# Kernel tuning notes

Measured on AMD Instinct MI355X. Metric: run time of the kernel, lower is better.

## Reference

```python
import jax, jax.numpy as jnp
import numpy as np

ITER_ROUTING = 3
FINAL_LAMBDA = 0.01
EPS = 1e-9

N = 4
CHILD_SPACE = 12
KERNEL = 3
STRIDE = 1
CHILD_CAPS = 16
PARENT_CAPS = 32
POSE = 16


def _routing_map(child_space, k, s):
    # (child_space^2, parent_space^2) binary map: child c feeds parent p.
    parent_space = (child_space - k) // s + 1
    m = np.zeros((child_space * child_space, parent_space * parent_space), np.float32)
    for pr in range(parent_space):
        for pc in range(parent_space):
            p = pr * parent_space + pc
            for r in range(k):
                for c in range(k):
                    m[(pr * s + r) * child_space + (pc * s + c), p] = 1.0
    return m


def setup_inputs() -> dict:
    key = jax.random.key(0)
    k1, k2, k3, k4 = jax.random.split(key, 4)
    parent_space = (CHILD_SPACE - KERNEL) // STRIDE + 1
    kk = KERNEL * KERNEL
    votes = jax.random.normal(k1, (N * parent_space * parent_space, kk * CHILD_CAPS, PARENT_CAPS, POSE), jnp.float32)
    acts = jax.random.uniform(k2, (N * parent_space * parent_space, kk * CHILD_CAPS, 1), dtype=jnp.float32)
    beta_v = jax.random.normal(k3, (1, 1, 1, 1, PARENT_CAPS, 1), jnp.float32)
    beta_a = jax.random.normal(k4, (1, 1, 1, 1, PARENT_CAPS, 1), jnp.float32)
    srm = jnp.asarray(_routing_map(CHILD_SPACE, KERNEL, STRIDE))
    return {"votes_ij": votes, "activations_i": acts, "beta_v": beta_v, "beta_a": beta_a,
            "spatial_routing_matrix": srm, "batch_size": N, "kk": kk}


def _em_routing(votes_ij, activations_i, beta_v, beta_a, srm, batch_size, kk):
    Nb = batch_size
    C2, P2 = srm.shape  # child_space^2, parent_space^2
    P = int(round(P2 ** 0.5))
    K_total, O, ch = votes_ij.shape[1], votes_ij.shape[2], votes_ij.shape[3]
    child_caps = K_total // kk

    votes = votes_ij.reshape(Nb, P, P, K_total, O, ch)
    act_i = activations_i.reshape(Nb, P, P, K_total, 1, 1)

    # children per parent, ascending child index (stable argsort on -1/0 values)
    cidx = jnp.argsort(-srm, axis=0)[:kk].T           # (P2, kk)
    seg = cidx.reshape(-1)                            # (P2*kk,) child id per (parent, slot)
    ppc = jnp.sum(srm, axis=1)                        # parents-per-child, (C2,)
    # init_rr: 1 / (parents_per_child * parent_caps + 1e-9), gathered per parent slot
    rr0 = (1.0 / (ppc[cidx] * O + 1e-9)).reshape(1, P, P, kk, 1, 1)
    rr = jnp.broadcast_to(rr0, (1, P, P, kk, child_caps, O)).reshape(1, P, P, K_total, O, 1)

    layer_norm_factor = 100.0 / (float(K_total) / float(O))

    def m_step(rr, it):
        lam = FINAL_LAMBDA * (1.0 - 0.95 ** (it + 1))
        rr_prime = rr * act_i                                            # (N,P,P,K,O,1)
        rr_prime_sum = jnp.sum(rr_prime, axis=-3, keepdims=True)         # (N,P,P,1,O,1)
        mean_j = jnp.sum(rr_prime * votes, axis=-3, keepdims=True) / (rr_prime_sum + EPS)
        var_j = jnp.sum(rr_prime * jnp.square(votes - mean_j), axis=-3, keepdims=True) / (rr_prime_sum + EPS)
        cost_j_h = (beta_v + 0.5 * jnp.log(var_j + EPS)) * rr_prime_sum * layer_norm_factor
        cost_j = jnp.sum(cost_j_h, axis=-1, keepdims=True)               # (N,P,P,1,O,1)
        cost_mean = jnp.mean(cost_j, axis=-2, keepdims=True)
        cost_stdv = jnp.sqrt(jnp.sum(jnp.square(cost_j - cost_mean), axis=-2, keepdims=True) / O)
        act_j = jax.nn.sigmoid(lam * (beta_a + (cost_mean - cost_j) / (cost_stdv + EPS)))
        return act_j, mean_j, var_j

    def e_step(act_j, mean_j, var_j):
        # log N(vote; mean_j, var_j) per parent + log activation
        o_p0 = -jnp.sum(jnp.square(votes - mean_j) / (2.0 * var_j), axis=-1, keepdims=True)
        o_p2 = -0.5 * jnp.sum(jnp.log(2.0 * np.pi * var_j), axis=-1, keepdims=True)
        zz = jnp.log(act_j + EPS) + o_p0 + o_p2                          # (N,P,P,K,O,1)
        # softmax over ALL parents of each child (spatial kk slots x parent_caps),
        # done via segment reductions keyed by child id (== sparse/softmax/dense of original)
        z = jnp.moveaxis(zz.reshape(Nb, P2 * kk, child_caps, O), 1, 0)   # (P2*kk, N, cc, O)
        m = jax.ops.segment_max(jnp.max(z, axis=-1), seg, num_segments=C2)  # (C2, N, cc)
        m = jnp.where(jnp.isinf(m), 0.0, m)
        e = jnp.exp(z - m[seg][..., None])
        denom = jax.ops.segment_sum(jnp.sum(e, axis=-1), seg, num_segments=C2)
        rr_new = e / denom[seg][..., None]
        return jnp.moveaxis(rr_new, 0, 1).reshape(Nb, P, P, K_total, O, 1)

    for it in range(ITER_ROUTING):
        act_j, mean_j, var_j = m_step(rr, it)
        if it < ITER_ROUTING - 1:
            rr = e_step(act_j, mean_j, var_j)

    poses_j = mean_j[:, :, :, 0]        # (N,P,P,O,16)
    activations_j = act_j[:, :, :, 0]   # (N,P,P,O,1)
    return poses_j, activations_j


def reference(votes_ij, activations_i, beta_v, beta_a, spatial_routing_matrix, batch_size, kk):
    return _em_routing(votes_ij, activations_i, beta_v, beta_a, spatial_routing_matrix, batch_size, kk)
```

## Files before the change

### kernel.cpp

```cpp
#include <hip/hip_runtime.h>
#include <math.h>

#define NB     4
#define P      10
#define P2     100
#define CS     12
#define CCAPS  16
#define KTOT   144
#define O      32
#define POSE   16
#define EPSF   1e-9f
#define LNF    22.2222222222222222f
#define LOG2PI 1.83787706640934548f

#define RRN (NB*P2*KTOT*O)

__device__ float g_rr[RRN];
__device__ float g_zz[RRN];

__device__ __forceinline__ int npar(int x) {
    int a = x + 1, b = CS - x;
    int m = a < 3 ? a : 3;
    return m < b ? m : b;
}

template<bool FIRST, bool LAST>
__global__ __launch_bounds__(512)
void mstep_kernel(const float* __restrict__ votes,
                  const float* __restrict__ acts,
                  const float* __restrict__ beta_v,
                  const float* __restrict__ beta_a,
                  float* __restrict__ out, float lam)
{
    __shared__ __align__(16) float rr_lds[KTOT * O];
    __shared__ float act_lds[KTOT];
    __shared__ __align__(16) float mean_lds[512];
    __shared__ __align__(16) float i2v_lds[512];
    __shared__ float cost_lds[O];
    __shared__ float slv_lds[O];
    __shared__ float zpre_lds[O];
    __shared__ float actj_lds[O];

    const int tid = threadIdx.x;
    const int kq  = tid >> 7;
    const int q   = tid & 127;
    const int o   = q >> 2;
    const int c4  = q & 3;
    const int bp  = blockIdx.x;
    const int p   = bp % P2;
    const int pr  = p / P, pc = p % P;

    if (tid < KTOT) act_lds[tid] = acts[bp * KTOT + tid];
    __syncthreads();

    if (FIRST) {
        for (int f = tid; f < KTOT * O / 4; f += 512) {
            int k = f >> 3;
            int kslot = k >> 4;
            int kr = kslot / 3, kc = kslot % 3;
            float ppc = (float)(npar(pr + kr) * npar(pc + kc));
            float r = act_lds[k] / (ppc * 32.0f + EPSF);
            ((float4*)rr_lds)[f] = make_float4(r, r, r, r);
        }
    } else {
        const float4* src = (const float4*)(g_rr + (size_t)bp * (KTOT * O));
        for (int f = tid; f < KTOT * O / 4; f += 512) {
            float4 r4 = src[f];
            float a = act_lds[f >> 3];
            r4.x *= a; r4.y *= a; r4.z *= a; r4.w *= a;
            ((float4*)rr_lds)[f] = r4;
        }
    }
    __syncthreads();

    const float* vb = votes + (size_t)bp * (KTOT * O * POSE);
    float  s  = 0.f;
    float4 m1 = make_float4(0.f, 0.f, 0.f, 0.f);
    float4 m2 = make_float4(0.f, 0.f, 0.f, 0.f);
    #pragma unroll 4
    for (int k = kq; k < KTOT; k += 4) {
        float  rp = rr_lds[k * O + o];
        float4 v  = *(const float4*)(vb + k * 512 + q * 4);
        s += rp;
        m1.x += rp * v.x;       m1.y += rp * v.y;
        m1.z += rp * v.z;       m1.w += rp * v.w;
        m2.x += rp * v.x * v.x; m2.y += rp * v.y * v.y;
        m2.z += rp * v.z * v.z; m2.w += rp * v.w * v.w;
    }
    __syncthreads();

    float4* lm1 = (float4*)rr_lds;
    float4* lm2 = (float4*)(rr_lds + 2048);
    float*  lss = rr_lds + 4096;
    lm1[tid] = m1; lm2[tid] = m2; lss[tid] = s;
    __syncthreads();

    if (tid < 128) {
        float4 a, b;
        a = lm1[tid];        b = lm1[128 + tid];
        m1.x = a.x + b.x; m1.y = a.y + b.y; m1.z = a.z + b.z; m1.w = a.w + b.w;
        a = lm1[256 + tid];  b = lm1[384 + tid];
        m1.x += a.x + b.x; m1.y += a.y + b.y; m1.z += a.z + b.z; m1.w += a.w + b.w;
        a = lm2[tid];        b = lm2[128 + tid];
        m2.x = a.x + b.x; m2.y = a.y + b.y; m2.z = a.z + b.z; m2.w = a.w + b.w;
        a = lm2[256 + tid];  b = lm2[384 + tid];
        m2.x += a.x + b.x; m2.y += a.y + b.y; m2.z += a.z + b.z; m2.w += a.w + b.w;
        s = lss[tid] + lss[128 + tid] + lss[256 + tid] + lss[384 + tid];

        float denom = s + EPSF;
        float4 mean, var, i2;
        mean.x = m1.x / denom; mean.y = m1.y / denom;
        mean.z = m1.z / denom; mean.w = m1.w / denom;
        var.x = m2.x / denom - mean.x * mean.x;
        var.y = m2.y / denom - mean.y * mean.y;
        var.z = m2.z / denom - mean.z * mean.z;
        var.w = m2.w / denom - mean.w * mean.w;
        var.x = fmaxf(var.x, 1e-30f); var.y = fmaxf(var.y, 1e-30f);
        var.z = fmaxf(var.z, 1e-30f); var.w = fmaxf(var.w, 1e-30f);
        i2.x = 0.5f / var.x; i2.y = 0.5f / var.y;
        i2.z = 0.5f / var.z; i2.w = 0.5f / var.w;
        ((float4*)mean_lds)[tid] = mean;
        ((float4*)i2v_lds)[tid]  = i2;

        float lv = logf(var.x + EPSF) + logf(var.y + EPSF)
                 + logf(var.z + EPSF) + logf(var.w + EPSF);
        float slv = lv;
        slv += __shfl_xor(slv, 1);
        slv += __shfl_xor(slv, 2);
        if (c4 == 0) {
            cost_lds[o] = (16.f * beta_v[o] + 0.5f * slv) * s * LNF;
            slv_lds[o]  = slv;
        }
    }
    __syncthreads();

    if (tid < 128) {
        float cm = 0.f;
        #pragma unroll
        for (int i = 0; i < O; ++i) cm += cost_lds[i];
        cm *= (1.0f / 32.0f);
        float sq = 0.f;
        #pragma unroll
        for (int i = 0; i < O; ++i) { float d = cost_lds[i] - cm; sq += d * d; }
        float cstd = sqrtf(sq * (1.0f / 32.0f));
        float aj = 1.f / (1.f + expf(-lam * (beta_a[o] + (cm - cost_lds[o]) / (cstd + EPSF))));
        if (c4 == 0) {
            actj_lds[o] = aj;
            zpre_lds[o] = logf(aj + EPSF) - 0.5f * (16.f * LOG2PI + slv_lds[o]);
        }
    }
    __syncthreads();

    if (LAST) {
        if (tid < 128)
            ((float4*)out)[bp * 128 + tid] = ((float4*)mean_lds)[tid];
        if (tid < O)
            out[(size_t)NB * P2 * 512 + bp * O + tid] = actj_lds[tid];
        return;
    }

    {
        float4 mean = ((float4*)mean_lds)[q];
        float4 i2   = ((float4*)i2v_lds)[q];
        float  zp   = zpre_lds[o];
        float* zzb  = g_zz + (size_t)bp * (KTOT * O);
        #pragma unroll 4
        for (int k = kq; k < KTOT; k += 4) {
            float4 v = *(const float4*)(vb + k * 512 + q * 4);
            float dx = v.x - mean.x, dy = v.y - mean.y;
            float dz = v.z - mean.z, dw = v.w - mean.w;
            float t = dx * dx * i2.x + dy * dy * i2.y + dz * dz * i2.z + dw * dw * i2.w;
            t += __shfl_xor(t, 1);
            t += __shfl_xor(t, 2);
            if (c4 == 0) zzb[k * O + o] = zp - t;
        }
    }
}

__global__ __launch_bounds__(512)
void estep_kernel()
{
    const int tid = threadIdx.x;
    const int bc  = blockIdx.x;
    const int b   = bc / (CS * CS);
    const int c   = bc % (CS * CS);
    const int cr  = c / CS, cl = c % CS;
    const int cc  = tid >> 5;
    const int o   = tid & 31;

    float vals[9];
    float vmax = -1e30f;
    #pragma unroll
    for (int kr = 0; kr < 3; ++kr) {
        int pr = cr - kr;
        #pragma unroll
        for (int kc = 0; kc < 3; ++kc) {
            int pc = cl - kc;
            float v = -1e30f;
            if (pr >= 0 && pr <= 9 && pc >= 0 && pc <= 9) {
                int pp = pr * P + pc;
                int kslot = kr * 3 + kc;
                size_t idx = ((size_t)(b * P2 + pp) * KTOT + kslot * CCAPS + cc) * O + o;
                v = g_zz[idx];
            }
            vals[kr * 3 + kc] = v;
            vmax = fmaxf(vmax, v);
        }
    }
    vmax = fmaxf(vmax, __shfl_xor(vmax, 1));
    vmax = fmaxf(vmax, __shfl_xor(vmax, 2));
    vmax = fmaxf(vmax, __shfl_xor(vmax, 4));
    vmax = fmaxf(vmax, __shfl_xor(vmax, 8));
    vmax = fmaxf(vmax, __shfl_xor(vmax, 16));

    float psum = 0.f;
    #pragma unroll
    for (int i = 0; i < 9; ++i) {
        float e = (vals[i] > -1e29f) ? expf(vals[i] - vmax) : 0.f;
        vals[i] = e;
        psum += e;
    }
    psum += __shfl_xor(psum, 1);
    psum += __shfl_xor(psum, 2);
    psum += __shfl_xor(psum, 4);
    psum += __shfl_xor(psum, 8);
    psum += __shfl_xor(psum, 16);
    float inv = 1.0f / psum;

    #pragma unroll
    for (int kr = 0; kr < 3; ++kr) {
        int pr = cr - kr;
        #pragma unroll
        for (int kc = 0; kc < 3; ++kc) {
            int pc = cl - kc;
            if (pr >= 0 && pr <= 9 && pc >= 0 && pc <= 9) {
                int pp = pr * P + pc;
                int kslot = kr * 3 + kc;
                size_t idx = ((size_t)(b * P2 + pp) * KTOT + kslot * CCAPS + cc) * O + o;
                g_rr[idx] = vals[kr * 3 + kc] * inv;
            }
        }
    }
}

extern "C" void kernel_launch(void* const* d_in, const int* in_sizes, int n_in,
                              void* d_out, int out_size, void* d_ws, size_t ws_size,
                              hipStream_t stream)
{
    (void)in_sizes; (void)n_in; (void)out_size; (void)d_ws; (void)ws_size;

    const float* votes = (const float*)d_in[0];
    const float* acts  = (const float*)d_in[1];
    const float* bv    = (const float*)d_in[2];
    const float* ba    = (const float*)d_in[3];
    float* out = (float*)d_out;

    const float lam0 = 0.01f * (1.0f - 0.95f);
    const float lam1 = 0.01f * (1.0f - 0.95f * 0.95f);
    const float lam2 = 0.01f * (1.0f - 0.95f * 0.95f * 0.95f);

    dim3 blk(512);
    mstep_kernel<true,  false><<<dim3(NB * P2), blk, 0, stream>>>(votes, acts, bv, ba, out, lam0);
    estep_kernel<<<dim3(NB * CS * CS), blk, 0, stream>>>();
    mstep_kernel<false, false><<<dim3(NB * P2), blk, 0, stream>>>(votes, acts, bv, ba, out, lam1);
    estep_kernel<<<dim3(NB * CS * CS), blk, 0, stream>>>();
    mstep_kernel<false, true ><<<dim3(NB * P2), blk, 0, stream>>>(votes, acts, bv, ba, out, lam2);
}
```

Before: 267.9 us.

## Split m-step into K-partitioned stats and finish kernels, fuse zz into e-step

The m-step is split into a stats kernel that runs four blocks per parent, each handling a quarter of the children, and a small finish kernel that combines the partial sums and computes mean, variance and activation. The Gaussian log-likelihood is no longer computed in the m-step and staged through g_zz. The e-step instead recomputes it from votes, mean and inverse variance, and the e-step grid is split four ways by child capsule. This raises block-level parallelism on the 400-block grid and removes one global round trip, at the cost of more kernel launches, partial-sum traffic, and an uncoalesced per-thread 64-byte read of votes in the e-step.

```diff
diff --git a/kernel.cpp b/kernel.cpp
--- a/kernel.cpp
+++ b/kernel.cpp
@@ -9,14 +9,21 @@
 #define KTOT   144
 #define O      32
 #define POSE   16
+#define VSZ    73728
 #define EPSF   1e-9f
 #define LNF    22.2222222222222222f
-#define LOG2PI 1.83787706640934548f
-
-#define RRN (NB*P2*KTOT*O)
-
-__device__ float g_rr[RRN];
-__device__ float g_zz[RRN];
+#define TWO_PI 6.28318530717958647f
+
+#define NBP    (NB*P2)
+#define RRN    (NBP*KTOT*O)
+
+__device__ float g_rr  [RRN];
+__device__ float g_m1  [NBP*4*512];
+__device__ float g_m2  [NBP*4*512];
+__device__ float g_s   [NBP*4*32];
+__device__ float g_mean[NBP*512];
+__device__ float g_i2v [NBP*512];
+__device__ float g_zpre[NBP*32];
 
 __device__ __forceinline__ int npar(int x) {
     int a = x + 1, b = CS - x;
@@ -24,187 +31,201 @@
     return m < b ? m : b;
 }
 
-template<bool FIRST, bool LAST>
+template<bool FIRST>
 __global__ __launch_bounds__(512)
-void mstep_kernel(const float* __restrict__ votes,
-                  const float* __restrict__ acts,
-                  const float* __restrict__ beta_v,
-                  const float* __restrict__ beta_a,
-                  float* __restrict__ out, float lam)
-{
-    __shared__ __align__(16) float rr_lds[KTOT * O];
-    __shared__ float act_lds[KTOT];
-    __shared__ __align__(16) float mean_lds[512];
-    __shared__ __align__(16) float i2v_lds[512];
-    __shared__ float cost_lds[O];
-    __shared__ float slv_lds[O];
-    __shared__ float zpre_lds[O];
-    __shared__ float actj_lds[O];
+void stats_kernel(const float* __restrict__ votes,
+                  const float* __restrict__ acts)
+{
+    __shared__ __align__(16) float rrp[36 * 32];
+    __shared__ float act_lds[36];
+    __shared__ __align__(16) float lm1[512 * 4];
+    __shared__ __align__(16) float lm2[512 * 4];
+    __shared__ float lss[512];
 
     const int tid = threadIdx.x;
-    const int kq  = tid >> 7;
+    const int ks  = tid >> 7;
     const int q   = tid & 127;
     const int o   = q >> 2;
-    const int c4  = q & 3;
-    const int bp  = blockIdx.x;
+    const int blk = blockIdx.x;
+    const int bp  = blk >> 2;
+    const int kq  = blk & 3;
     const int p   = bp % P2;
     const int pr  = p / P, pc = p % P;
-
-    if (tid < KTOT) act_lds[tid] = acts[bp * KTOT + tid];
-    __syncthreads();
-
-    if (FIRST) {
-        for (int f = tid; f < KTOT * O / 4; f += 512) {
-            int k = f >> 3;
-            int kslot = k >> 4;
+    const int k0  = kq * 36;
+
+    if (tid < 36) act_lds[tid] = acts[bp * KTOT + k0 + tid];
+    __syncthreads();
+
+    if (tid < 288) {
+        int kk = tid >> 3;
+        float4 r4;
+        if (FIRST) {
+            int ka = k0 + kk;
+            int kslot = ka >> 4;
             int kr = kslot / 3, kc = kslot % 3;
             float ppc = (float)(npar(pr + kr) * npar(pc + kc));
-            float r = act_lds[k] / (ppc * 32.0f + EPSF);
-            ((float4*)rr_lds)[f] = make_float4(r, r, r, r);
+            float r = act_lds[kk] / (ppc * 32.0f + EPSF);
+            r4 = make_float4(r, r, r, r);
+        } else {
+            r4 = ((const float4*)(g_rr + (size_t)bp * (KTOT * O) + k0 * 32))[tid];
+            float a = act_lds[kk];
+            r4.x *= a; r4.y *= a; r4.z *= a; r4.w *= a;
         }
-    } else {
-        const float4* src = (const float4*)(g_rr + (size_t)bp * (KTOT * O));
-        for (int f = tid; f < KTOT * O / 4; f += 512) {
-            float4 r4 = src[f];
-            float a = act_lds[f >> 3];
-            r4.x *= a; r4.y *= a; r4.z *= a; r4.w *= a;
-            ((float4*)rr_lds)[f] = r4;
-        }
-    }
-    __syncthreads();
-
-    const float* vb = votes + (size_t)bp * (KTOT * O * POSE);
+        ((float4*)rrp)[tid] = r4;
+    }
+    __syncthreads();
+
+    const float* vb = votes + (size_t)bp * VSZ;
     float  s  = 0.f;
     float4 m1 = make_float4(0.f, 0.f, 0.f, 0.f);
     float4 m2 = make_float4(0.f, 0.f, 0.f, 0.f);
-    #pragma unroll 4
-    for (int k = kq; k < KTOT; k += 4) {
-        float  rp = rr_lds[k * O + o];
-        float4 v  = *(const float4*)(vb + k * 512 + q * 4);
+    const int kl0 = ks * 9;
+    #pragma unroll
+    for (int i = 0; i < 9; ++i) {
+        float  rp = rrp[(kl0 + i) * 32 + o];
+        float4 v  = *(const float4*)(vb + (k0 + kl0 + i) * 512 + q * 4);
         s += rp;
         m1.x += rp * v.x;       m1.y += rp * v.y;
         m1.z += rp * v.z;       m1.w += rp * v.w;
         m2.x += rp * v.x * v.x; m2.y += rp * v.y * v.y;
         m2.z += rp * v.z * v.z; m2.w += rp * v.w * v.w;
     }
-    __syncthreads();
-
-    float4* lm1 = (float4*)rr_lds;
-    float4* lm2 = (float4*)(rr_lds + 2048);
-    float*  lss = rr_lds + 4096;
-    lm1[tid] = m1; lm2[tid] = m2; lss[tid] = s;
+
+    ((float4*)lm1)[tid] = m1;
+    ((float4*)lm2)[tid] = m2;
+    lss[tid] = s;
     __syncthreads();
 
     if (tid < 128) {
         float4 a, b;
-        a = lm1[tid];        b = lm1[128 + tid];
+        a = ((float4*)lm1)[tid];       b = ((float4*)lm1)[tid + 128];
         m1.x = a.x + b.x; m1.y = a.y + b.y; m1.z = a.z + b.z; m1.w = a.w + b.w;
-        a = lm1[256 + tid];  b = lm1[384 + tid];
+        a = ((float4*)lm1)[tid + 256]; b = ((float4*)lm1)[tid + 384];
         m1.x += a.x + b.x; m1.y += a.y + b.y; m1.z += a.z + b.z; m1.w += a.w + b.w;
-        a = lm2[tid];        b = lm2[128 + tid];
+        a = ((float4*)lm2)[tid];       b = ((float4*)lm2)[tid + 128];
         m2.x = a.x + b.x; m2.y = a.y + b.y; m2.z = a.z + b.z; m2.w = a.w + b.w;
-        a = lm2[256 + tid];  b = lm2[384 + tid];
+        a = ((float4*)lm2)[tid + 256]; b = ((float4*)lm2)[tid + 384];
         m2.x += a.x + b.x; m2.y += a.y + b.y; m2.z += a.z + b.z; m2.w += a.w + b.w;
-        s = lss[tid] + lss[128 + tid] + lss[256 + tid] + lss[384 + tid];
-
-        float denom = s + EPSF;
-        float4 mean, var, i2;
-        mean.x = m1.x / denom; mean.y = m1.y / denom;
-        mean.z = m1.z / denom; mean.w = m1.w / denom;
-        var.x = m2.x / denom - mean.x * mean.x;
-        var.y = m2.y / denom - mean.y * mean.y;
-        var.z = m2.z / denom - mean.z * mean.z;
-        var.w = m2.w / denom - mean.w * mean.w;
-        var.x = fmaxf(var.x, 1e-30f); var.y = fmaxf(var.y, 1e-30f);
-        var.z = fmaxf(var.z, 1e-30f); var.w = fmaxf(var.w, 1e-30f);
-        i2.x = 0.5f / var.x; i2.y = 0.5f / var.y;
-        i2.z = 0.5f / var.z; i2.w = 0.5f / var.w;
-        ((float4*)mean_lds)[tid] = mean;
-        ((float4*)i2v_lds)[tid]  = i2;
-
-        float lv = logf(var.x + EPSF) + logf(var.y + EPSF)
-                 + logf(var.z + EPSF) + logf(var.w + EPSF);
-        float slv = lv;
-        slv += __shfl_xor(slv, 1);
-        slv += __shfl_xor(slv, 2);
-        if (c4 == 0) {
-            cost_lds[o] = (16.f * beta_v[o] + 0.5f * slv) * s * LNF;
-            slv_lds[o]  = slv;
-        }
-    }
-    __syncthreads();
-
-    if (tid < 128) {
-        float cm = 0.f;
-        #pragma unroll
-        for (int i = 0; i < O; ++i) cm += cost_lds[i];
-        cm *= (1.0f / 32.0f);
-        float sq = 0.f;
-        #pragma unroll
-        for (int i = 0; i < O; ++i) { float d = cost_lds[i] - cm; sq += d * d; }
-        float cstd = sqrtf(sq * (1.0f / 32.0f));
-        float aj = 1.f / (1.f + expf(-lam * (beta_a[o] + (cm - cost_lds[o]) / (cstd + EPSF))));
-        if (c4 == 0) {
-            actj_lds[o] = aj;
-            zpre_lds[o] = logf(aj + EPSF) - 0.5f * (16.f * LOG2PI + slv_lds[o]);
-        }
-    }
-    __syncthreads();
+        s = lss[tid] + lss[tid + 128] + lss[tid + 256] + lss[tid + 384];
+
+        ((float4*)g_m1)[blk * 128 + tid] = m1;
+        ((float4*)g_m2)[blk * 128 + tid] = m2;
+        if ((tid & 3) == 0) g_s[blk * 32 + (tid >> 2)] = s;
+    }
+}
+
+template<bool LAST>
+__global__ __launch_bounds__(128)
+void finish_kernel(const float* __restrict__ beta_v,
+                   const float* __restrict__ beta_a,
+                   float* __restrict__ out, float lam)
+{
+    __shared__ float cost_lds[O];
+
+    const int tid = threadIdx.x;
+    const int o   = tid >> 2;
+    const int c4  = tid & 3;
+    const int bp  = blockIdx.x;
+
+    float4 m1 = make_float4(0.f, 0.f, 0.f, 0.f);
+    float4 m2 = make_float4(0.f, 0.f, 0.f, 0.f);
+    float  s  = 0.f;
+    #pragma unroll
+    for (int kq = 0; kq < 4; ++kq) {
+        float4 a = ((const float4*)g_m1)[(bp * 4 + kq) * 128 + tid];
+        float4 b = ((const float4*)g_m2)[(bp * 4 + kq) * 128 + tid];
+        m1.x += a.x; m1.y += a.y; m1.z += a.z; m1.w += a.w;
+        m2.x += b.x; m2.y += b.y; m2.z += b.z; m2.w += b.w;
+        s += g_s[(bp * 4 + kq) * 32 + o];
+    }
+
+    float denom = s + EPSF;
+    float4 mean, var, i2;
+    mean.x = m1.x / denom; mean.y = m1.y / denom;
+    mean.z = m1.z / denom; mean.w = m1.w / denom;
+    var.x = fmaxf(m2.x / denom - mean.x * mean.x, 1e-30f);
+    var.y = fmaxf(m2.y / denom - mean.y * mean.y, 1e-30f);
+    var.z = fmaxf(m2.z / denom - mean.z * mean.z, 1e-30f);
+    var.w = fmaxf(m2.w / denom - mean.w * mean.w, 1e-30f);
+    i2.x = 0.5f / var.x; i2.y = 0.5f / var.y;
+    i2.z = 0.5f / var.z; i2.w = 0.5f / var.w;
+
+    float lve = logf(var.x + EPSF) + logf(var.y + EPSF)
+              + logf(var.z + EPSF) + logf(var.w + EPSF);
+    float lv2 = logf(TWO_PI * var.x) + logf(TWO_PI * var.y)
+              + logf(TWO_PI * var.z) + logf(TWO_PI * var.w);
+    lve += __shfl_xor(lve, 1); lve += __shfl_xor(lve, 2);
+    lv2 += __shfl_xor(lv2, 1); lv2 += __shfl_xor(lv2, 2);
+
+    if (c4 == 0)
+        cost_lds[o] = (16.f * beta_v[o] + 0.5f * lve) * s * LNF;
+    __syncthreads();
+
+    float cm = 0.f;
+    #pragma unroll
+    for (int i = 0; i < O; ++i) cm += cost_lds[i];
+    cm *= (1.0f / 32.0f);
+    float sq = 0.f;
+    #pragma unroll
+    for (int i = 0; i < O; ++i) { float d = cost_lds[i] - cm; sq += d * d; }
+    float cstd = sqrtf(sq * (1.0f / 32.0f));
+    float aj = 1.f / (1.f + expf(-lam * (beta_a[o] + (cm - cost_lds[o]) / (cstd + EPSF))));
 
     if (LAST) {
-        if (tid < 128)
-            ((float4*)out)[bp * 128 + tid] = ((float4*)mean_lds)[tid];
-        if (tid < O)
-            out[(size_t)NB * P2 * 512 + bp * O + tid] = actj_lds[tid];
-        return;
-    }
-
-    {
-        float4 mean = ((float4*)mean_lds)[q];
-        float4 i2   = ((float4*)i2v_lds)[q];
-        float  zp   = zpre_lds[o];
-        float* zzb  = g_zz + (size_t)bp * (KTOT * O);
-        #pragma unroll 4
-        for (int k = kq; k < KTOT; k += 4) {
-            float4 v = *(const float4*)(vb + k * 512 + q * 4);
-            float dx = v.x - mean.x, dy = v.y - mean.y;
-            float dz = v.z - mean.z, dw = v.w - mean.w;
-            float t = dx * dx * i2.x + dy * dy * i2.y + dz * dz * i2.z + dw * dw * i2.w;
-            t += __shfl_xor(t, 1);
-            t += __shfl_xor(t, 2);
-            if (c4 == 0) zzb[k * O + o] = zp - t;
-        }
-    }
-}
-
-__global__ __launch_bounds__(512)
-void estep_kernel()
+        ((float4*)out)[bp * 128 + tid] = mean;
+        if (c4 == 0) out[(size_t)NBP * 512 + bp * 32 + o] = aj;
+    } else {
+        ((float4*)g_mean)[bp * 128 + tid] = mean;
+        ((float4*)g_i2v)[bp * 128 + tid]  = i2;
+        if (c4 == 0) g_zpre[bp * 32 + o] = logf(aj + EPSF) - 0.5f * lv2;
+    }
+}
+
+__global__ __launch_bounds__(128)
+void estep_kernel(const float* __restrict__ votes)
 {
     const int tid = threadIdx.x;
-    const int bc  = blockIdx.x;
+    const int o   = tid & 31;
+    const int ccl = tid >> 5;
+    const int blk = blockIdx.x;
+    const int ccq = blk & 3;
+    const int bc  = blk >> 2;
     const int b   = bc / (CS * CS);
     const int c   = bc % (CS * CS);
     const int cr  = c / CS, cl = c % CS;
-    const int cc  = tid >> 5;
-    const int o   = tid & 31;
-
-    float vals[9];
+    const int cc  = ccq * 4 + ccl;
+
+    float zz[9];
     float vmax = -1e30f;
     #pragma unroll
     for (int kr = 0; kr < 3; ++kr) {
-        int pr = cr - kr;
+        int prr = cr - kr;
         #pragma unroll
         for (int kc = 0; kc < 3; ++kc) {
-            int pc = cl - kc;
-            float v = -1e30f;
-            if (pr >= 0 && pr <= 9 && pc >= 0 && pc <= 9) {
-                int pp = pr * P + pc;
-                int kslot = kr * 3 + kc;
-                size_t idx = ((size_t)(b * P2 + pp) * KTOT + kslot * CCAPS + cc) * O + o;
-                v = g_zz[idx];
+            int pcc = cl - kc;
+            int si = kr * 3 + kc;
+            float z = -1e30f;
+            if (prr >= 0 && prr <= 9 && pcc >= 0 && pcc <= 9) {
+                int bpp = b * P2 + prr * P + pcc;
+                const float* st = g_mean + bpp * 512 + o * 16;
+                const float* iv = g_i2v  + bpp * 512 + o * 16;
+                const float* vv = votes + (size_t)bpp * VSZ
+                                  + (si * CCAPS + cc) * 512 + o * 16;
+                float t = 0.f;
+                #pragma unroll
+                for (int j = 0; j < 4; ++j) {
+                    float4 v = *(const float4*)(vv + j * 4);
+                    float4 m = *(const float4*)(st + j * 4);
+                    float4 w = *(const float4*)(iv + j * 4);
+                    float dx = v.x - m.x, dy = v.y - m.y;
+                    float dz = v.z - m.z, dw = v.w - m.w;
+                    t += dx * dx * w.x + dy * dy * w.y
+                       + dz * dz * w.z + dw * dw * w.w;
+                }
+                z = g_zpre[bpp * 32 + o] - t;
             }
-            vals[kr * 3 + kc] = v;
-            vmax = fmaxf(vmax, v);
+            zz[si] = z;
+            vmax = fmaxf(vmax, z);
         }
     }
     vmax = fmaxf(vmax, __shfl_xor(vmax, 1));
@@ -213,31 +234,31 @@
     vmax = fmaxf(vmax, __shfl_xor(vmax, 8));
     vmax = fmaxf(vmax, __shfl_xor(vmax, 16));
 
-    float psum = 0.f;
-    #pragma unroll
-    for (int i = 0; i < 9; ++i) {
-        float e = (vals[i] > -1e29f) ? expf(vals[i] - vmax) : 0.f;
-        vals[i] = e;
-        psum += e;
-    }
-    psum += __shfl_xor(psum, 1);
-    psum += __shfl_xor(psum, 2);
-    psum += __shfl_xor(psum, 4);
-    psum += __shfl_xor(psum, 8);
-    psum += __shfl_xor(psum, 16);
-    float inv = 1.0f / psum;
+    float ps = 0.f;
+    #pragma unroll
+    for (int si = 0; si < 9; ++si) {
+        float e = (zz[si] > -1e29f) ? expf(zz[si] - vmax) : 0.f;
+        zz[si] = e;
+        ps += e;
+    }
+    ps += __shfl_xor(ps, 1);
+    ps += __shfl_xor(ps, 2);
+    ps += __shfl_xor(ps, 4);
+    ps += __shfl_xor(ps, 8);
+    ps += __shfl_xor(ps, 16);
+    float inv = 1.0f / ps;
 
     #pragma unroll
     for (int kr = 0; kr < 3; ++kr) {
-        int pr = cr - kr;
+        int prr = cr - kr;
         #pragma unroll
         for (int kc = 0; kc < 3; ++kc) {
-            int pc = cl - kc;
-            if (pr >= 0 && pr <= 9 && pc >= 0 && pc <= 9) {
-                int pp = pr * P + pc;
-                int kslot = kr * 3 + kc;
-                size_t idx = ((size_t)(b * P2 + pp) * KTOT + kslot * CCAPS + cc) * O + o;
-                g_rr[idx] = vals[kr * 3 + kc] * inv;
+            int pcc = cl - kc;
+            int si = kr * 3 + kc;
+            if (prr >= 0 && prr <= 9 && pcc >= 0 && pcc <= 9) {
+                int bpp = b * P2 + prr * P + pcc;
+                g_rr[(size_t)bpp * (KTOT * O) + (si * CCAPS + cc) * 32 + o]
+                    = zz[si] * inv;
             }
         }
     }
@@ -259,10 +280,14 @@
     const float lam1 = 0.01f * (1.0f - 0.95f * 0.95f);
     const float lam2 = 0.01f * (1.0f - 0.95f * 0.95f * 0.95f);
 
-    dim3 blk(512);
-    mstep_kernel<true,  false><<<dim3(NB * P2), blk, 0, stream>>>(votes, acts, bv, ba, out, lam0);
-    estep_kernel<<<dim3(NB * CS * CS), blk, 0, stream>>>();
-    mstep_kernel<false, false><<<dim3(NB * P2), blk, 0, stream>>>(votes, acts, bv, ba, out, lam1);
-    estep_kernel<<<dim3(NB * CS * CS), blk, 0, stream>>>();
-    mstep_kernel<false, true ><<<dim3(NB * P2), blk, 0, stream>>>(votes, acts, bv, ba, out, lam2);
-}
+    stats_kernel<true ><<<dim3(NBP * 4), dim3(512), 0, stream>>>(votes, acts);
+    finish_kernel<false><<<dim3(NBP), dim3(128), 0, stream>>>(bv, ba, out, lam0);
+    estep_kernel<<<dim3(NB * CS * CS * 4), dim3(128), 0, stream>>>(votes);
+
+    stats_kernel<false><<<dim3(NBP * 4), dim3(512), 0, stream>>>(votes, acts);
+    finish_kernel<false><<<dim3(NBP), dim3(128), 0, stream>>>(bv, ba, out, lam1);
+    estep_kernel<<<dim3(NB * CS * CS * 4), dim3(128), 0, stream>>>(votes);
+
+    stats_kernel<false><<<dim3(NBP * 4), dim3(512), 0, stream>>>(votes, acts);
+    finish_kernel<true ><<<dim3(NBP), dim3(128), 0, stream>>>(bv, ba, out, lam2);
+}
```

Measured after the change: 288.4 us. 1.08x slower.
